# Kernel tuning notes

Measured on AMD Instinct MI355X. Metric: run time of the kernel, lower is better.

## Reference

```python
import jax, jax.numpy as jnp
import numpy as np

N = 200000   # nodes
K = 16       # fixed neighbor count per node
D = 8        # per-node value dim


def setup_inputs() -> dict:
    key = jax.random.key(0)
    k1, k2, k3, k4 = jax.random.split(key, 4)
    values = jax.random.normal(k1, (N, D), dtype=jnp.float32)
    neighbor_idx = jax.random.randint(k2, (N, K), 0, N, dtype=jnp.int64)
    # per-node Linear(K*D -> D): weight [N, K*D, D], bias [N, D]
    W = jax.random.normal(k3, (N, K * D, D), dtype=jnp.float32) * (1.0 / np.sqrt(K * D))
    b = jax.random.normal(k4, (N, D), dtype=jnp.float32) * 0.01
    return {"values": values, "neighbor_idx": neighbor_idx, "W": W, "b": b}


def reference(values, neighbor_idx, W, b):
    # gather each node's neighbor values and concat along feature dim:
    # values[neighbor_idx] -> [N, K, D] -> [N, K*D]
    gathered = values[neighbor_idx].reshape(values.shape[0], -1)
    # per-node tiny linear: out[n] = gathered[n] @ W[n] + b[n]
    pre = jnp.einsum('nf,nfd->nd', gathered, W) + b
    return jax.nn.sigmoid(pre)
```

## Files before the change

kernel.cpp:

```cpp
#include <hip/hip_runtime.h>

#define N_NODES 200000
#define K 16
#define D 8

__global__ __launch_bounds__(256) void node_linear_sigmoid(
    const float* __restrict__ values,
    const int*   __restrict__ nbr,
    const float* __restrict__ W,
    const float* __restrict__ bias,
    float*       __restrict__ out)
{
    const int tid = blockIdx.x * blockDim.x + threadIdx.x;
    if (tid >= N_NODES * 2) return;
    const int n = tid >> 1;
    const int h = tid & 1;

    const float4* __restrict__ W4 = (const float4*)W + (size_t)n * 256 + h;
    const int*    __restrict__ my_nbr = nbr + n * K;

    float4 acc = make_float4(0.f, 0.f, 0.f, 0.f);

    #pragma unroll 2
    for (int k = 0; k < K; ++k) {
        const int s = my_nbr[k];
        const float4* __restrict__ v4 = (const float4*)(values + (size_t)s * D);
        const float4 v0 = v4[0];
        const float4 v1 = v4[1];
        const float g[8] = {v0.x, v0.y, v0.z, v0.w, v1.x, v1.y, v1.z, v1.w};
        const float4* __restrict__ Wk = W4 + k * 16;
        #pragma unroll
        for (int j = 0; j < 8; ++j) {
            const float4 w = Wk[(size_t)j * 2];
            acc.x = fmaf(g[j], w.x, acc.x);
            acc.y = fmaf(g[j], w.y, acc.y);
            acc.z = fmaf(g[j], w.z, acc.z);
            acc.w = fmaf(g[j], w.w, acc.w);
        }
    }

    const float4 bb = *((const float4*)(bias + (size_t)n * D) + h);
    acc.x += bb.x; acc.y += bb.y; acc.z += bb.z; acc.w += bb.w;

    float4 r;
    r.x = 1.f / (1.f + __expf(-acc.x));
    r.y = 1.f / (1.f + __expf(-acc.y));
    r.z = 1.f / (1.f + __expf(-acc.z));
    r.w = 1.f / (1.f + __expf(-acc.w));

    *((float4*)(out + (size_t)n * D) + h) = r;
}

extern "C" void kernel_launch(void* const* d_in, const int* in_sizes, int n_in,
                              void* d_out, int out_size, void* d_ws, size_t ws_size,
                              hipStream_t stream) {
    const float* values = (const float*)d_in[0];
    const int*   nbr    = (const int*)d_in[1];
    const float* W      = (const float*)d_in[2];
    const float* bias   = (const float*)d_in[3];
    float*       out    = (float*)d_out;

    const int total_threads = N_NODES * 2;
    const int block = 256;
    const int grid = (total_threads + block - 1) / block;
    node_linear_sigmoid<<<grid, block, 0, stream>>>(values, nbr, W, bias, out);
}
```

Before: 1.094 ms.

## Assign one wavefront per node for coalesced weight streaming with shuffle reduction

```diff
diff --git a/kernel.cpp b/kernel.cpp
--- a/kernel.cpp
+++ b/kernel.cpp
@@ -4,51 +4,57 @@
 #define K 16
 #define D 8
 
-__global__ __launch_bounds__(256) void node_linear_sigmoid(
+typedef float vfloat4 __attribute__((ext_vector_type(4)));
+
+__global__ __launch_bounds__(256) void node_linear_sigmoid_wave(
     const float* __restrict__ values,
     const int*   __restrict__ nbr,
     const float* __restrict__ W,
     const float* __restrict__ bias,
     float*       __restrict__ out)
 {
-    const int tid = blockIdx.x * blockDim.x + threadIdx.x;
-    if (tid >= N_NODES * 2) return;
-    const int n = tid >> 1;
-    const int h = tid & 1;
+    __shared__ float g[4][128];
+    const int lane = threadIdx.x & 63;
+    const int wave = threadIdx.x >> 6;
+    const int n = blockIdx.x * 4 + wave;
 
-    const float4* __restrict__ W4 = (const float4*)W + (size_t)n * 256 + h;
-    const int*    __restrict__ my_nbr = nbr + n * K;
+    const int k = lane >> 2;
+    const int c = lane & 3;
+    const int s = nbr[n * K + k];
+    const float2 v = *(const float2*)(values + (size_t)s * D + c * 2);
+    *(float2*)&g[wave][2 * lane] = v;
+    __syncthreads();
 
-    float4 acc = make_float4(0.f, 0.f, 0.f, 0.f);
-
-    #pragma unroll 2
-    for (int k = 0; k < K; ++k) {
-        const int s = my_nbr[k];
-        const float4* __restrict__ v4 = (const float4*)(values + (size_t)s * D);
-        const float4 v0 = v4[0];
-        const float4 v1 = v4[1];
-        const float g[8] = {v0.x, v0.y, v0.z, v0.w, v1.x, v1.y, v1.z, v1.w};
-        const float4* __restrict__ Wk = W4 + k * 16;
-        #pragma unroll
-        for (int j = 0; j < 8; ++j) {
-            const float4 w = Wk[(size_t)j * 2];
-            acc.x = fmaf(g[j], w.x, acc.x);
-            acc.y = fmaf(g[j], w.y, acc.y);
-            acc.z = fmaf(g[j], w.z, acc.z);
-            acc.w = fmaf(g[j], w.w, acc.w);
-        }
+    const vfloat4* __restrict__ W4 = (const vfloat4*)W + (size_t)n * 256;
+    const int half = lane >> 1;
+    vfloat4 p = {0.f, 0.f, 0.f, 0.f};
+    #pragma unroll
+    for (int t = 0; t < 4; ++t) {
+        const vfloat4 w4 = __builtin_nontemporal_load(W4 + t * 64 + lane);
+        const float gf = g[wave][32 * t + half];
+        p.x = fmaf(gf, w4.x, p.x);
+        p.y = fmaf(gf, w4.y, p.y);
+        p.z = fmaf(gf, w4.z, p.z);
+        p.w = fmaf(gf, w4.w, p.w);
     }
 
-    const float4 bb = *((const float4*)(bias + (size_t)n * D) + h);
-    acc.x += bb.x; acc.y += bb.y; acc.z += bb.z; acc.w += bb.w;
+    #pragma unroll
+    for (int m = 2; m <= 32; m <<= 1) {
+        p.x += __shfl_xor(p.x, m, 64);
+        p.y += __shfl_xor(p.y, m, 64);
+        p.z += __shfl_xor(p.z, m, 64);
+        p.w += __shfl_xor(p.w, m, 64);
+    }
 
-    float4 r;
-    r.x = 1.f / (1.f + __expf(-acc.x));
-    r.y = 1.f / (1.f + __expf(-acc.y));
-    r.z = 1.f / (1.f + __expf(-acc.z));
-    r.w = 1.f / (1.f + __expf(-acc.w));
-
-    *((float4*)(out + (size_t)n * D) + h) = r;
+    if (lane < 2) {
+        const vfloat4 bb = ((const vfloat4*)(bias + (size_t)n * D))[lane];
+        vfloat4 r;
+        r.x = 1.f / (1.f + __expf(-(p.x + bb.x)));
+        r.y = 1.f / (1.f + __expf(-(p.y + bb.y)));
+        r.z = 1.f / (1.f + __expf(-(p.z + bb.z)));
+        r.w = 1.f / (1.f + __expf(-(p.w + bb.w)));
+        ((vfloat4*)(out + (size_t)n * D))[lane] = r;
+    }
 }
 
 extern "C" void kernel_launch(void* const* d_in, const int* in_sizes, int n_in,
@@ -60,8 +66,7 @@
     const float* bias   = (const float*)d_in[3];
     float*       out    = (float*)d_out;
 
-    const int total_threads = N_NODES * 2;
     const int block = 256;
-    const int grid = (total_threads + block - 1) / block;
-    node_linear_sigmoid<<<grid, block, 0, stream>>>(values, nbr, W, bias, out);
+    const int grid = N_NODES / 4;
+    node_linear_sigmoid_wave<<<grid, block, 0, stream>>>(values, nbr, W, bias, out);
 }
```

Result: faster. 1.014 ms (-7.4%).
